# Performance work log

Hardware: AMD Instinct MI355X
Metric: run time of the kernel (lower is better)

Reference implementation:

```python
import jax, jax.numpy as jnp
import numpy as np

B, S, D, F, H, E = 4, 1024, 512, 2048, 8, 8
LN_EPS = 1e-5


def setup_inputs() -> dict:
    key = jax.random.key(0)
    ks = jax.random.split(key, 8)
    sd = 1.0 / np.sqrt(D)
    return {
        'x': jax.random.normal(ks[0], (B, S, D), jnp.float32),
        'in_proj_w': jax.random.normal(ks[1], (3 * D, D), jnp.float32) * sd,
        'in_proj_b': jnp.zeros((3 * D,), jnp.float32),
        'out_proj_w': jax.random.normal(ks[2], (D, D), jnp.float32) * sd,
        'out_proj_b': jnp.zeros((D,), jnp.float32),
        'ln1_g': jnp.ones((D,), jnp.float32),
        'ln1_b': jnp.zeros((D,), jnp.float32),
        'ln2_g': jnp.ones((D,), jnp.float32),
        'ln2_b': jnp.zeros((D,), jnp.float32),
        'router_w': jax.random.normal(ks[3], (D, E), jnp.float32) * sd,
        'wi': jax.random.normal(ks[4], (E, D, F), jnp.float32) * sd,
        'wo': jax.random.normal(ks[5], (E, F, D), jnp.float32) * (1.0 / np.sqrt(F)),
        'expert_capacity': 256,
    }


def _layernorm(x, g, b):
    mu = jnp.mean(x, axis=-1, keepdims=True)
    var = jnp.var(x, axis=-1, keepdims=True)
    return (x - mu) * jax.lax.rsqrt(var + LN_EPS) * g + b


def _mha(x, in_w, in_b, out_w, out_b):
    # torch nn.MultiheadAttention, batch_first, self-attention, no mask
    qkv = x @ in_w.T + in_b                         # [B,S,3D]
    q, k, v = jnp.split(qkv, 3, axis=-1)
    hd = D // H

    def heads(t):
        return t.reshape(B, S, H, hd).transpose(0, 2, 1, 3)  # [B,H,S,hd]

    q, k, v = heads(q), heads(k), heads(v)
    scores = jnp.einsum('bhqd,bhkd->bhqk', q, k) / np.sqrt(hd)
    attn = jax.nn.softmax(scores, axis=-1)
    o = jnp.einsum('bhqk,bhkd->bhqd', attn, v)
    o = o.transpose(0, 2, 1, 3).reshape(B, S, D)
    return o @ out_w.T + out_b


def _router(x, router_w, capacity):
    # Switch-style top-1 router with per-(batch,expert) capacity
    logits = x.astype(jnp.float32) @ router_w       # [B,S,E]
    probs = jax.nn.softmax(logits, axis=-1)
    idx = jnp.argmax(probs, axis=-1)                # [B,S]
    one_hot = jax.nn.one_hot(idx, E, dtype=probs.dtype)
    pos = jnp.cumsum(one_hot, axis=1)               # position within each expert queue
    keep = one_hot * (pos <= capacity).astype(probs.dtype)
    expert_mask = keep * probs                      # dispatch mask scaled by router prob
    return expert_mask, probs, logits


def reference(x, in_proj_w, in_proj_b, out_proj_w, out_proj_b,
              ln1_g, ln1_b, ln2_g, ln2_b, router_w, wi, wo, expert_capacity):
    # self-attention block (post-norm)
    residual = x
    a = _mha(x, in_proj_w, in_proj_b, out_proj_w, out_proj_b)
    h = _layernorm(residual + a, ln1_g, ln1_b)

    # sparse MoE FFN
    expert_mask, _, router_logits = _router(h, router_w, expert_capacity)
    residual = h
    moe = jnp.zeros_like(h)
    for e in range(E):  # fixed small expert loop; masked-dense == gather/FFN/scatter
        y = jax.nn.gelu(h @ wi[e], approximate=False) @ wo[e]
        moe = moe + expert_mask[..., e:e + 1] * y

    out = _layernorm(residual + moe, ln2_g, ln2_b)
    return out, router_logits, expert_mask
```

## Files before the change

kernel.cpp:

```cpp
#include <hip/hip_runtime.h>
#include <math.h>

#define SEQ 1024
#define NTOK 4096
#define DM 512
#define FF 2048
#define NE 8

typedef __attribute__((ext_vector_type(8))) short bf16x8;
typedef __attribute__((ext_vector_type(4))) float f32x4;

__device__ __forceinline__ short f2bf(float f) {
  unsigned u = __float_as_uint(f);
  unsigned r = (u + 0x7FFFu + ((u >> 16) & 1u)) >> 16;
  return (short)r;
}
__device__ __forceinline__ float bf2f(short h) {
  return __uint_as_float(((unsigned)(unsigned short)h) << 16);
}

#define GLOAD_LDS16(g, l) __builtin_amdgcn_global_load_lds( \
    (const __attribute__((address_space(1))) void*)(g),     \
    (__attribute__((address_space(3))) void*)(l), 16, 0, 0)

__global__ __launch_bounds__(256) void split_kernel(const float* __restrict__ src,
    short* __restrict__ hi, short* __restrict__ lo) {
  const size_t base = ((size_t)blockIdx.x * 256 + threadIdx.x) * 8;
  float4 v0 = *reinterpret_cast<const float4*>(src + base);
  float4 v1 = *reinterpret_cast<const float4*>(src + base + 4);
  short h[8]; short l[8];
  float v[8] = {v0.x, v0.y, v0.z, v0.w, v1.x, v1.y, v1.z, v1.w};
#pragma unroll
  for (int i = 0; i < 8; ++i) {
    h[i] = f2bf(v[i]);
    l[i] = f2bf(v[i] - bf2f(h[i]));
  }
  *reinterpret_cast<short4*>(hi + base)     = make_short4(h[0], h[1], h[2], h[3]);
  *reinterpret_cast<short4*>(hi + base + 4) = make_short4(h[4], h[5], h[6], h[7]);
  *reinterpret_cast<short4*>(lo + base)     = make_short4(l[0], l[1], l[2], l[3]);
  *reinterpret_cast<short4*>(lo + base + 4) = make_short4(l[4], l[5], l[6], l[7]);
}

template<int BNF>
__global__ __launch_bounds__(256) void gemm_split(const short* __restrict__ Ah, const short* __restrict__ Al,
    const short* __restrict__ Bh, const short* __restrict__ Bl,
    const float* __restrict__ bias, const float* __restrict__ resid, float* __restrict__ C,
    int N, int K) {
  constexpr int BN = 32 * BNF;
  __shared__ __align__(16) short AsH[128 * 32];
  __shared__ __align__(16) short AsL[128 * 32];
  __shared__ __align__(16) short BsH[BN * 32];
  __shared__ __align__(16) short BsL[BN * 32];
  const int n0 = blockIdx.x * BN, m0 = blockIdx.y * 128;
  const int tid = threadIdx.x;
  const int lane = tid & 63, w = tid >> 6;
  const int quad = lane >> 4, l15 = lane & 15;
  const int wm = (w & 1) * 64, wn = (w >> 1) * 16 * BNF;
  const int sr = tid >> 2, sc = (tid & 3) * 8;
  const short* Ahp = Ah + (size_t)(m0 + sr) * K;
  const short* Alp = Al + (size_t)(m0 + sr) * K;
  const short* Bhp = Bh + (size_t)(n0 + sr) * K;
  const short* Blp = Bl + (size_t)(n0 + sr) * K;
  f32x4 acc[4][BNF];
#pragma unroll
  for (int i = 0; i < 4; ++i)
#pragma unroll
    for (int j = 0; j < BNF; ++j) acc[i][j] = (f32x4){0.f, 0.f, 0.f, 0.f};
  for (int kt = 0; kt < K; kt += 32) {
    GLOAD_LDS16(Ahp + kt + sc,                  &AsH[tid * 8]);
    GLOAD_LDS16(Ahp + (size_t)64 * K + kt + sc, &AsH[2048 + tid * 8]);
    GLOAD_LDS16(Alp + kt + sc,                  &AsL[tid * 8]);
    GLOAD_LDS16(Alp + (size_t)64 * K + kt + sc, &AsL[2048 + tid * 8]);
    GLOAD_LDS16(Bhp + kt + sc,                  &BsH[tid * 8]);
    GLOAD_LDS16(Blp + kt + sc,                  &BsL[tid * 8]);
    if (BNF == 4) {
      GLOAD_LDS16(Bhp + (size_t)64 * K + kt + sc, &BsH[2048 + tid * 8]);
      GLOAD_LDS16(Blp + (size_t)64 * K + kt + sc, &BsL[2048 + tid * 8]);
    }
    __syncthreads();
    bf16x8 ah[4], al[4], bh[BNF], bl[BNF];
#pragma unroll
    for (int i = 0; i < 4; ++i) {
      ah[i] = *reinterpret_cast<const bf16x8*>(&AsH[(wm + i * 16 + l15) * 32 + quad * 8]);
      al[i] = *reinterpret_cast<const bf16x8*>(&AsL[(wm + i * 16 + l15) * 32 + quad * 8]);
    }
#pragma unroll
    for (int j = 0; j < BNF; ++j) {
      bh[j] = *reinterpret_cast<const bf16x8*>(&BsH[(wn + j * 16 + l15) * 32 + quad * 8]);
      bl[j] = *reinterpret_cast<const bf16x8*>(&BsL[(wn + j * 16 + l15) * 32 + quad * 8]);
    }
#pragma unroll
    for (int i = 0; i < 4; ++i)
#pragma unroll
      for (int j = 0; j < BNF; ++j) {
        acc[i][j] = __builtin_amdgcn_mfma_f32_16x16x32_bf16(al[i], bh[j], acc[i][j], 0, 0, 0);
        acc[i][j] = __builtin_amdgcn_mfma_f32_16x16x32_bf16(ah[i], bl[j], acc[i][j], 0, 0, 0);
        acc[i][j] = __builtin_amdgcn_mfma_f32_16x16x32_bf16(ah[i], bh[j], acc[i][j], 0, 0, 0);
      }
    __syncthreads();
  }
#pragma unroll
  for (int i = 0; i < 4; ++i) {
#pragma unroll
    for (int reg = 0; reg < 4; ++reg) {
      const int row = m0 + wm + i * 16 + quad * 4 + reg;
#pragma unroll
      for (int j = 0; j < BNF; ++j) {
        const int col = n0 + wn + j * 16 + l15;
        float v = acc[i][j][reg] + bias[col];
        if (resid) v += resid[(size_t)row * N + col];
        C[(size_t)row * N + col] = v;
      }
    }
  }
}

__global__ __launch_bounds__(256) void gemm_split_qkv(const short* __restrict__ Ah, const short* __restrict__ Al,
    const short* __restrict__ Bh, const short* __restrict__ Bl, const float* __restrict__ bias,
    short* __restrict__ qkh, short* __restrict__ qkl, short* __restrict__ vh, short* __restrict__ vl) {
  const int K = DM;
  __shared__ __align__(16) short AsH[128 * 32];
  __shared__ __align__(16) short AsL[128 * 32];
  __shared__ __align__(16) short BsH[64 * 32];
  __shared__ __align__(16) short BsL[64 * 32];
  const int n0 = blockIdx.x * 64, m0 = blockIdx.y * 128;
  const int tid = threadIdx.x;
  const int lane = tid & 63, w = tid >> 6;
  const int quad = lane >> 4, l15 = lane & 15;
  const int wm = (w & 1) * 64, wn = (w >> 1) * 32;
  const int sr = tid >> 2, sc = (tid & 3) * 8;
  const short* Ahp = Ah + (size_t)(m0 + sr) * K;
  const short* Alp = Al + (size_t)(m0 + sr) * K;
  const short* Bhp = Bh + (size_t)(n0 + sr) * K;
  const short* Blp = Bl + (size_t)(n0 + sr) * K;
  f32x4 acc[4][2];
#pragma unroll
  for (int i = 0; i < 4; ++i)
#pragma unroll
    for (int j = 0; j < 2; ++j) acc[i][j] = (f32x4){0.f, 0.f, 0.f, 0.f};
  for (int kt = 0; kt < K; kt += 32) {
    GLOAD_LDS16(Ahp + kt + sc,                  &AsH[tid * 8]);
    GLOAD_LDS16(Ahp + (size_t)64 * K + kt + sc, &AsH[2048 + tid * 8]);
    GLOAD_LDS16(Alp + kt + sc,                  &AsL[tid * 8]);
    GLOAD_LDS16(Alp + (size_t)64 * K + kt + sc, &AsL[2048 + tid * 8]);
    GLOAD_LDS16(Bhp + kt + sc,                  &BsH[tid * 8]);
    GLOAD_LDS16(Blp + kt + sc,                  &BsL[tid * 8]);
    __syncthreads();
    bf16x8 ah[4], al[4], bh[2], bl[2];
#pragma unroll
    for (int i = 0; i < 4; ++i) {
      ah[i] = *reinterpret_cast<const bf16x8*>(&AsH[(wm + i * 16 + l15) * 32 + quad * 8]);
      al[i] = *reinterpret_cast<const bf16x8*>(&AsL[(wm + i * 16 + l15) * 32 + quad * 8]);
    }
#pragma unroll
    for (int j = 0; j < 2; ++j) {
      bh[j] = *reinterpret_cast<const bf16x8*>(&BsH[(wn + j * 16 + l15) * 32 + quad * 8]);
      bl[j] = *reinterpret_cast<const bf16x8*>(&BsL[(wn + j * 16 + l15) * 32 + quad * 8]);
    }
#pragma unroll
    for (int i = 0; i < 4; ++i)
#pragma unroll
      for (int j = 0; j < 2; ++j) {
        acc[i][j] = __builtin_amdgcn_mfma_f32_16x16x32_bf16(al[i], bh[j], acc[i][j], 0, 0, 0);
        acc[i][j] = __builtin_amdgcn_mfma_f32_16x16x32_bf16(ah[i], bl[j], acc[i][j], 0, 0, 0);
        acc[i][j] = __builtin_amdgcn_mfma_f32_16x16x32_bf16(ah[i], bh[j], acc[i][j], 0, 0, 0);
      }
    __syncthreads();
  }
  if (n0 < 1024) {
#pragma unroll
    for (int i = 0; i < 4; ++i) {
#pragma unroll
      for (int reg = 0; reg < 4; ++reg) {
        const int row = m0 + wm + i * 16 + quad * 4 + reg;
#pragma unroll
        for (int j = 0; j < 2; ++j) {
          const int col = n0 + wn + j * 16 + l15;
          float v = acc[i][j][reg] + bias[col];
          short hv = f2bf(v);
          size_t ad = (size_t)row * 1024 + col;
          qkh[ad] = hv;
          qkl[ad] = f2bf(v - bf2f(hv));
        }
      }
    }
  } else {
#pragma unroll
    for (int i = 0; i < 4; ++i) {
      const int row0 = m0 + wm + i * 16 + quad * 4;
      const int bb = row0 >> 10, s0 = row0 & 1023;
#pragma unroll
      for (int j = 0; j < 2; ++j) {
        const int col = n0 + wn + j * 16 + l15;
        const int c2 = col - 1024;
        const int hhd = c2 >> 6, d = c2 & 63;
        const float bc = bias[col];
        float v0 = acc[i][j][0] + bc, v1 = acc[i][j][1] + bc, v2 = acc[i][j][2] + bc, v3 = acc[i][j][3] + bc;
        short4 hv = make_short4(f2bf(v0), f2bf(v1), f2bf(v2), f2bf(v3));
        short4 lv = make_short4(f2bf(v0 - bf2f(hv.x)), f2bf(v1 - bf2f(hv.y)),
                                f2bf(v2 - bf2f(hv.z)), f2bf(v3 - bf2f(hv.w)));
        size_t ad = ((size_t)(bb * 8 + hhd) * 64 + d) * 1024 + s0;
        *reinterpret_cast<short4*>(vh + ad) = hv;
        *reinterpret_cast<short4*>(vl + ad) = lv;
      }
    }
  }
}

__global__ __launch_bounds__(256) void attn_mfma(const short* __restrict__ qkh, const short* __restrict__ qkl,
    const short* __restrict__ vth, const short* __restrict__ vtl,
    float* __restrict__ opart, float* __restrict__ ml) {
  const int qt = blockIdx.x, hh = blockIdx.y;
  const int b = blockIdx.z >> 1, ks = blockIdx.z & 1;
  __shared__ __align__(16) short Qh[4096], Ql[4096], Kh[4096], Kl[4096], Vh[4096], Vl[4096];
  const int tid = threadIdx.x;
  const int lane = tid & 63, w = tid >> 6;
  const int quad = lane >> 4, l15 = lane & 15;
  const int tok0 = b * SEQ + qt * 64;
  const int srow = tid >> 2, schunk = (tid & 3) * 8;
  {
    const size_t qa = (size_t)(tok0 + srow) * 1024 + hh * 64 + schunk;
    GLOAD_LDS16(qkh + qa,      &Qh[tid * 8]);
    GLOAD_LDS16(qkh + qa + 32, &Qh[2048 + tid * 8]);
    GLOAD_LDS16(qkl + qa,      &Ql[tid * 8]);
    GLOAD_LDS16(qkl + qa + 32, &Ql[2048 + tid * 8]);
  }
  __syncthreads();
  bf16x8 qfh[2], qfl[2];
#pragma unroll
  for (int kk = 0; kk < 2; ++kk) {
    qfh[kk] = *reinterpret_cast<const bf16x8*>(&Qh[kk * 2048 + (w * 16 + l15) * 32 + quad * 8]);
    qfl[kk] = *reinterpret_cast<const bf16x8*>(&Ql[kk * 2048 + (w * 16 + l15) * 32 + quad * 8]);
  }
  f32x4 oacc[4];
  float m_run[4], l_run[4];
#pragma unroll
  for (int r = 0; r < 4; ++r) { oacc[r] = (f32x4){0.f, 0.f, 0.f, 0.f}; m_run[r] = -1e30f; l_run[r] = 0.f; }
  const size_t kbase = (size_t)(b * SEQ) * 1024 + 512 + hh * 64;
  const size_t vbase = (size_t)(b * 8 + hh) * 64 * 1024;
  for (int kc = ks * 8; kc < ks * 8 + 8; ++kc) {
    const size_t ka = kbase + (size_t)(kc * 64 + srow) * 1024 + schunk;
    GLOAD_LDS16(qkh + ka,      &Kh[tid * 8]);
    GLOAD_LDS16(qkh + ka + 32, &Kh[2048 + tid * 8]);
    GLOAD_LDS16(qkl + ka,      &Kl[tid * 8]);
    GLOAD_LDS16(qkl + ka + 32, &Kl[2048 + tid * 8]);
    const size_t va = vbase + (size_t)srow * 1024 + kc * 64 + schunk;
    GLOAD_LDS16(vth + va,      &Vh[tid * 8]);
    GLOAD_LDS16(vth + va + 32, &Vh[2048 + tid * 8]);
    GLOAD_LDS16(vtl + va,      &Vl[tid * 8]);
    GLOAD_LDS16(vtl + va + 32, &Vl[2048 + tid * 8]);
    __syncthreads();
    f32x4 s[4];
#pragma unroll
    for (int j = 0; j < 4; ++j) s[j] = (f32x4){0.f, 0.f, 0.f, 0.f};
#pragma unroll
    for (int kk = 0; kk < 2; ++kk)
#pragma unroll
      for (int j = 0; j < 4; ++j) {
        bf16x8 kfh = *reinterpret_cast<const bf16x8*>(&Kh[kk * 2048 + (j * 16 + l15) * 32 + quad * 8]);
        bf16x8 kfl = *reinterpret_cast<const bf16x8*>(&Kl[kk * 2048 + (j * 16 + l15) * 32 + quad * 8]);
        s[j] = __builtin_amdgcn_mfma_f32_16x16x32_bf16(qfl[kk], kfh, s[j], 0, 0, 0);
        s[j] = __builtin_amdgcn_mfma_f32_16x16x32_bf16(qfh[kk], kfl, s[j], 0, 0, 0);
        s[j] = __builtin_amdgcn_mfma_f32_16x16x32_bf16(qfh[kk], kfh, s[j], 0, 0, 0);
      }
    __syncthreads();
    float pv[4][4], alpha[4];
#pragma unroll
    for (int reg = 0; reg < 4; ++reg) {
      float mc = fmaxf(fmaxf(s[0][reg], s[1][reg]), fmaxf(s[2][reg], s[3][reg]));
#pragma unroll
      for (int msk = 1; msk < 16; msk <<= 1) mc = fmaxf(mc, __shfl_xor(mc, msk, 64));
      mc *= 0.125f;
      float mn = fmaxf(m_run[reg], mc);
      alpha[reg] = expf(m_run[reg] - mn);
      m_run[reg] = mn;
      float pl = 0.f;
#pragma unroll
      for (int j = 0; j < 4; ++j) { float pp = expf(s[j][reg] * 0.125f - mn); pv[j][reg] = pp; pl += pp; }
#pragma unroll
      for (int msk = 1; msk < 16; msk <<= 1) pl += __shfl_xor(pl, msk, 64);
      l_run[reg] = l_run[reg] * alpha[reg] + pl;
    }
#pragma unroll
    for (int j = 0; j < 4; ++j) {
      oacc[j][0] *= alpha[0]; oacc[j][1] *= alpha[1]; oacc[j][2] *= alpha[2]; oacc[j][3] *= alpha[3];
    }
#pragma unroll
    for (int j = 0; j < 4; ++j) {
      const int cad = (j >> 1) * 2048 + (j & 1) * 16 + l15;
#pragma unroll
      for (int reg = 0; reg < 4; ++reg) {
        const int ad = cad + (w * 16 + quad * 4 + reg) * 32;
        float p = pv[j][reg];
        short hp = f2bf(p);
        Kh[ad] = hp;
        Kl[ad] = f2bf(p - bf2f(hp));
      }
    }
#pragma unroll
    for (int kk = 0; kk < 2; ++kk) {
      bf16x8 pfh = *reinterpret_cast<const bf16x8*>(&Kh[kk * 2048 + (w * 16 + l15) * 32 + quad * 8]);
      bf16x8 pfl = *reinterpret_cast<const bf16x8*>(&Kl[kk * 2048 + (w * 16 + l15) * 32 + quad * 8]);
#pragma unroll
      for (int j = 0; j < 4; ++j) {
        bf16x8 vfh = *reinterpret_cast<const bf16x8*>(&Vh[kk * 2048 + (j * 16 + l15) * 32 + quad * 8]);
        bf16x8 vfl = *reinterpret_cast<const bf16x8*>(&Vl[kk * 2048 + (j * 16 + l15) * 32 + quad * 8]);
        oacc[j] = __builtin_amdgcn_mfma_f32_16x16x32_bf16(pfl, vfh, oacc[j], 0, 0, 0);
        oacc[j] = __builtin_amdgcn_mfma_f32_16x16x32_bf16(pfh, vfl, oacc[j], 0, 0, 0);
        oacc[j] = __builtin_amdgcn_mfma_f32_16x16x32_bf16(pfh, vfh, oacc[j], 0, 0, 0);
      }
    }
    __syncthreads();
  }
  float* op = opart + (size_t)ks * 2097152;
#pragma unroll
  for (int reg = 0; reg < 4; ++reg) {
    const int rloc = w * 16 + quad * 4 + reg;
#pragma unroll
    for (int j = 0; j < 4; ++j)
      op[(size_t)(tok0 + rloc) * 512 + hh * 64 + j * 16 + l15] = oacc[j][reg];
    if (l15 == 0) {
      size_t mli = (((size_t)ks * 32 + b * 8 + hh) * 1024 + qt * 64 + rloc) * 2;
      ml[mli] = m_run[reg];
      ml[mli + 1] = l_run[reg];
    }
  }
}

__global__ __launch_bounds__(64) void combine_attn(const float* __restrict__ opart, const float* __restrict__ ml,
    short* __restrict__ oh, short* __restrict__ ol) {
  const int t = blockIdx.x;
  const int b = t >> 10, s = t & 1023;
  const int tid = threadIdx.x;
#pragma unroll
  for (int hh = 0; hh < 8; ++hh) {
    size_t mli = (((size_t)(b * 8 + hh)) * 1024 + s) * 2;
    float m0 = ml[mli], l0 = ml[mli + 1];
    float m1 = ml[65536 + mli], l1 = ml[65536 + mli + 1];
    float mm = fmaxf(m0, m1);
    float a0 = expf(m0 - mm), a1 = expf(m1 - mm);
    float inv = 1.f / (l0 * a0 + l1 * a1);
    size_t ad = (size_t)t * 512 + hh * 64 + tid;
    float v = (opart[ad] * a0 + opart[2097152 + ad] * a1) * inv;
    short hv = f2bf(v);
    oh[ad] = hv;
    ol[ad] = f2bf(v - bf2f(hv));
  }
}

__global__ __launch_bounds__(64) void ln_router(const float* __restrict__ r1,
    const float* __restrict__ g, const float* __restrict__ bta, const float* __restrict__ rw,
    float* __restrict__ h, float* __restrict__ rlog, float* __restrict__ probs, int* __restrict__ am) {
  const int t = blockIdx.x, tid = threadIdx.x;
  const size_t base = (size_t)t * DM + tid * 8;
  float4 v0 = *reinterpret_cast<const float4*>(r1 + base);
  float4 v1 = *reinterpret_cast<const float4*>(r1 + base + 4);
  float s = v0.x+v0.y+v0.z+v0.w + v1.x+v1.y+v1.z+v1.w;
  float q = v0.x*v0.x+v0.y*v0.y+v0.z*v0.z+v0.w*v0.w + v1.x*v1.x+v1.y*v1.y+v1.z*v1.z+v1.w*v1.w;
#pragma unroll
  for (int m = 1; m < 64; m <<= 1) { s += __shfl_xor(s, m, 64); q += __shfl_xor(q, m, 64); }
  float mean = s * (1.0f/512.0f);
  float var = q * (1.0f/512.0f) - mean * mean;
  float rs = rsqrtf(var + 1e-5f);
  float4 g0 = *reinterpret_cast<const float4*>(g + tid*8);
  float4 g1 = *reinterpret_cast<const float4*>(g + tid*8 + 4);
  float4 b0 = *reinterpret_cast<const float4*>(bta + tid*8);
  float4 b1 = *reinterpret_cast<const float4*>(bta + tid*8 + 4);
  float hv[8];
  hv[0] = (v0.x-mean)*rs*g0.x+b0.x; hv[1] = (v0.y-mean)*rs*g0.y+b0.y;
  hv[2] = (v0.z-mean)*rs*g0.z+b0.z; hv[3] = (v0.w-mean)*rs*g0.w+b0.w;
  hv[4] = (v1.x-mean)*rs*g1.x+b1.x; hv[5] = (v1.y-mean)*rs*g1.y+b1.y;
  hv[6] = (v1.z-mean)*rs*g1.z+b1.z; hv[7] = (v1.w-mean)*rs*g1.w+b1.w;
  *reinterpret_cast<float4*>(h + base)     = make_float4(hv[0], hv[1], hv[2], hv[3]);
  *reinterpret_cast<float4*>(h + base + 4) = make_float4(hv[4], hv[5], hv[6], hv[7]);
  float lg[8] = {0.f,0.f,0.f,0.f,0.f,0.f,0.f,0.f};
  const float* rwp = rw + tid * 64;
#pragma unroll
  for (int r = 0; r < 8; ++r) {
    float4 w0 = *reinterpret_cast<const float4*>(rwp + r * 8);
    float4 w1 = *reinterpret_cast<const float4*>(rwp + r * 8 + 4);
    float hr = hv[r];
    lg[0] += hr * w0.x; lg[1] += hr * w0.y; lg[2] += hr * w0.z; lg[3] += hr * w0.w;
    lg[4] += hr * w1.x; lg[5] += hr * w1.y; lg[6] += hr * w1.z; lg[7] += hr * w1.w;
  }
#pragma unroll
  for (int m = 1; m < 64; m <<= 1) {
#pragma unroll
    for (int e = 0; e < 8; ++e) lg[e] += __shfl_xor(lg[e], m, 64);
  }
  int best = 0; float bv = lg[0];
#pragma unroll
  for (int e = 1; e < 8; ++e) if (lg[e] > bv) { bv = lg[e]; best = e; }
  float se = 0.f;
#pragma unroll
  for (int e = 0; e < 8; ++e) se += expf(lg[e] - bv);
  float inv = 1.f / se;
  if (tid < 8) {
    rlog[t * 8 + tid] = lg[tid];
    probs[t * 8 + tid] = expf(lg[tid] - bv) * inv;
  }
  if (tid == 0) am[t] = best;
}

__global__ __launch_bounds__(64) void ln2_kernel(const float* __restrict__ x, const float* __restrict__ add,
    const int* __restrict__ pos, const int* __restrict__ capp,
    const float* __restrict__ g, const float* __restrict__ bta, float* __restrict__ y) {
  const int t = blockIdx.x, tid = threadIdx.x;
  const size_t base = (size_t)t * DM + tid * 8;
  float4 v0 = *reinterpret_cast<const float4*>(x + base);
  float4 v1 = *reinterpret_cast<const float4*>(x + base + 4);
  if (pos[t] <= *capp) {
    float4 a0 = *reinterpret_cast<const float4*>(add + base);
    float4 a1 = *reinterpret_cast<const float4*>(add + base + 4);
    v0.x += a0.x; v0.y += a0.y; v0.z += a0.z; v0.w += a0.w;
    v1.x += a1.x; v1.y += a1.y; v1.z += a1.z; v1.w += a1.w;
  }
  float s = v0.x+v0.y+v0.z+v0.w + v1.x+v1.y+v1.z+v1.w;
  float q = v0.x*v0.x+v0.y*v0.y+v0.z*v0.z+v0.w*v0.w + v1.x*v1.x+v1.y*v1.y+v1.z*v1.z+v1.w*v1.w;
#pragma unroll
  for (int m = 1; m < 64; m <<= 1) { s += __shfl_xor(s, m, 64); q += __shfl_xor(q, m, 64); }
  float mean = s * (1.0f/512.0f);
  float var = q * (1.0f/512.0f) - mean * mean;
  float rs = rsqrtf(var + 1e-5f);
  float4 g0 = *reinterpret_cast<const float4*>(g + tid*8);
  float4 g1 = *reinterpret_cast<const float4*>(g + tid*8 + 4);
  float4 b0 = *reinterpret_cast<const float4*>(bta + tid*8);
  float4 b1 = *reinterpret_cast<const float4*>(bta + tid*8 + 4);
  float4 o0 = make_float4((v0.x-mean)*rs*g0.x+b0.x, (v0.y-mean)*rs*g0.y+b0.y,
                          (v0.z-mean)*rs*g0.z+b0.z, (v0.w-mean)*rs*g0.w+b0.w);
  float4 o1 = make_float4((v1.x-mean)*rs*g1.x+b1.x, (v1.y-mean)*rs*g1.y+b1.y,
                          (v1.z-mean)*rs*g1.z+b1.z, (v1.w-mean)*rs*g1.w+b1.w);
  *reinterpret_cast<float4*>(y + base) = o0;
  *reinterpret_cast<float4*>(y + base + 4) = o1;
}

__global__ __launch_bounds__(256) void scan_kernel(const int* __restrict__ am, const float* __restrict__ probs,
    const int* __restrict__ capp, float* __restrict__ emask, int* __restrict__ pos, int* __restrict__ cnt) {
  const int bx = blockIdx.x;
  const int b = bx >> 3, e = bx & 7;
  const int tid = threadIdx.x;
  const int cap = *capp;
  __shared__ int arr[256];
  const int s_base = tid * 4;
  int f[4], incl[4];
  int c = 0;
#pragma unroll
  for (int i = 0; i < 4; ++i) {
    f[i] = (am[b * SEQ + s_base + i] == e) ? 1 : 0;
    c += f[i]; incl[i] = c;
  }
  arr[tid] = c;
  __syncthreads();
  for (int off = 1; off < 256; off <<= 1) {
    int v = (tid >= off) ? arr[tid - off] : 0;
    __syncthreads();
    arr[tid] += v;
    __syncthreads();
  }
  int excl = arr[tid] - c;
  int tot = arr[255];
#pragma unroll
  for (int i = 0; i < 4; ++i) {
    int token = b * SEQ + s_base + i;
    int p = excl + incl[i];
    bool kept = f[i] && (p <= cap);
    emask[(size_t)token * NE + e] = kept ? probs[token * NE + e] : 0.f;
    if (f[i]) pos[token] = p;
  }
  if (tid == 0) cnt[bx] = (tot < cap) ? tot : cap;
}

__global__ __launch_bounds__(64) void offsets_kernel(const int* __restrict__ cnt, int* __restrict__ offbe,
    int* __restrict__ total) {
  int e = threadIdx.x;
  if (e < NE) {
    int run = 0;
    for (int b = 0; b < 4; ++b) { offbe[b * NE + e] = run; run += cnt[b * NE + e]; }
    total[e] = run;
  }
}

__global__ __launch_bounds__(256) void transpose_bf16(const float* __restrict__ W, short* __restrict__ Wt,
    int K, int N) {
  __shared__ float T[32][33];
  const float* We = W + (size_t)blockIdx.z * K * N;
  short* Wte = Wt + (size_t)blockIdx.z * K * N;
  const int k0 = blockIdx.y * 32, n0 = blockIdx.x * 32;
  const int r = threadIdx.x >> 3, c4 = (threadIdx.x & 7) * 4;
  float4 v = *reinterpret_cast<const float4*>(&We[(size_t)(k0 + r) * N + n0 + c4]);
  T[r][c4+0] = v.x; T[r][c4+1] = v.y; T[r][c4+2] = v.z; T[r][c4+3] = v.w;
  __syncthreads();
  short4 o;
  o.x = f2bf(T[c4+0][r]); o.y = f2bf(T[c4+1][r]); o.z = f2bf(T[c4+2][r]); o.w = f2bf(T[c4+3][r]);
  *reinterpret_cast<short4*>(&Wte[(size_t)(n0 + r) * K + k0 + c4]) = o;
}

__global__ __launch_bounds__(128) void gather_kernel(const float* __restrict__ h, const int* __restrict__ am,
    const int* __restrict__ pos, const int* __restrict__ capp, const int* __restrict__ offbe,
    const float* __restrict__ probs, short* __restrict__ Gb, int* __restrict__ tok, float* __restrict__ mscale) {
  const int t = blockIdx.x;
  const int b = t >> 10;
  const int e = am[t];
  const int p = pos[t];
  if (p > *capp) return;
  const int slot = offbe[b * NE + e] + p - 1;
  const int idx = e * 1024 + slot;
  if (threadIdx.x == 0) { tok[idx] = t; mscale[idx] = probs[t * NE + e]; }
  float4 v = *reinterpret_cast<const float4*>(h + (size_t)t * DM + threadIdx.x * 4);
  short4 o; o.x = f2bf(v.x); o.y = f2bf(v.y); o.z = f2bf(v.z); o.w = f2bf(v.w);
  *reinterpret_cast<short4*>(Gb + (size_t)idx * DM + threadIdx.x * 4) = o;
}

__global__ __launch_bounds__(256) void ffn1_mfma(const short* __restrict__ Gb, const short* __restrict__ wi_t,
    short* __restrict__ mid, const int* __restrict__ total) {
  const int e = blockIdx.z;
  const int tot = total[e];
  const int m0 = blockIdx.y * 128;
  if (m0 >= tot) return;
  const int n0 = blockIdx.x * 128;
  __shared__ __align__(16) short As[128 * 32];
  __shared__ __align__(16) short Bs[128 * 32];
  const short* A = Gb + ((size_t)e * 1024 + m0) * DM;
  const short* B = wi_t + (size_t)e * FF * DM + (size_t)n0 * DM;
  const int tid = threadIdx.x;
  const int lane = tid & 63, w = tid >> 6;
  const int quad = lane >> 4, l15 = lane & 15;
  const int wm = (w & 1) * 64, wn = (w >> 1) * 64;
  const int sr = tid >> 2, sc = (tid & 3) * 8;
  f32x4 acc[4][4];
#pragma unroll
  for (int i = 0; i < 4; ++i)
#pragma unroll
    for (int j = 0; j < 4; ++j) acc[i][j] = (f32x4){0.f, 0.f, 0.f, 0.f};
  for (int kt = 0; kt < DM; kt += 32) {
    GLOAD_LDS16(A + (size_t)sr * DM + kt + sc,        &As[tid * 8]);
    GLOAD_LDS16(A + (size_t)(sr + 64) * DM + kt + sc, &As[2048 + tid * 8]);
    GLOAD_LDS16(B + (size_t)sr * DM + kt + sc,        &Bs[tid * 8]);
    GLOAD_LDS16(B + (size_t)(sr + 64) * DM + kt + sc, &Bs[2048 + tid * 8]);
    __syncthreads();
    bf16x8 a[4], b[4];
#pragma unroll
    for (int i = 0; i < 4; ++i) a[i] = *reinterpret_cast<const bf16x8*>(&As[(wm + i * 16 + l15) * 32 + quad * 8]);
#pragma unroll
    for (int j = 0; j < 4; ++j) b[j] = *reinterpret_cast<const bf16x8*>(&Bs[(wn + j * 16 + l15) * 32 + quad * 8]);
#pragma unroll
    for (int i = 0; i < 4; ++i)
#pragma unroll
      for (int j = 0; j < 4; ++j)
        acc[i][j] = __builtin_amdgcn_mfma_f32_16x16x32_bf16(a[i], b[j], acc[i][j], 0, 0, 0);
    __syncthreads();
  }
#pragma unroll
  for (int i = 0; i < 4; ++i) {
#pragma unroll
    for (int reg = 0; reg < 4; ++reg) {
      int row = m0 + wm + i * 16 + quad * 4 + reg;
      short* outr = mid + ((size_t)e * 1024 + row) * FF;
#pragma unroll
      for (int j = 0; j < 4; ++j) {
        float v = acc[i][j][reg];
        float gl = 0.5f * v * (1.f + erff(v * 0.70710678118654752f));
        outr[n0 + wn + j * 16 + l15] = f2bf(gl);
      }
    }
  }
}

__global__ __launch_bounds__(256) void ffn2_mfma(const short* __restrict__ mid, const short* __restrict__ wo_t,
    const int* __restrict__ tok, const float* __restrict__ mscale, const int* __restrict__ total,
    float* __restrict__ moebuf) {
  const int e = blockIdx.z;
  const int tot = total[e];
  const int m0 = blockIdx.y * 128;
  if (m0 >= tot) return;
  const int n0 = blockIdx.x * 128;
  __shared__ __align__(16) short As[128 * 32];
  __shared__ __align__(16) short Bs[128 * 32];
  const short* A = mid + ((size_t)e * 1024 + m0) * FF;
  const short* B = wo_t + (size_t)e * DM * FF + (size_t)n0 * FF;
  const int tid = threadIdx.x;
  const int lane = tid & 63, w = tid >> 6;
  const int quad = lane >> 4, l15 = lane & 15;
  const int wm = (w & 1) * 64, wn = (w >> 1) * 64;
  const int sr = tid >> 2, sc = (tid & 3) * 8;
  f32x4 acc[4][4];
#pragma unroll
  for (int i = 0; i < 4; ++i)
#pragma unroll
    for (int j = 0; j < 4; ++j) acc[i][j] = (f32x4){0.f, 0.f, 0.f, 0.f};
  for (int kt = 0; kt < FF; kt += 32) {
    GLOAD_LDS16(A + (size_t)sr * FF + kt + sc,        &As[tid * 8]);
    GLOAD_LDS16(A + (size_t)(sr + 64) * FF + kt + sc, &As[2048 + tid * 8]);
    GLOAD_LDS16(B + (size_t)sr * FF + kt + sc,        &Bs[tid * 8]);
    GLOAD_LDS16(B + (size_t)(sr + 64) * FF + kt + sc, &Bs[2048 + tid * 8]);
    __syncthreads();
    bf16x8 a[4], b[4];
#pragma unroll
    for (int i = 0; i < 4; ++i) a[i] = *reinterpret_cast<const bf16x8*>(&As[(wm + i * 16 + l15) * 32 + quad * 8]);
#pragma unroll
    for (int j = 0; j < 4; ++j) b[j] = *reinterpret_cast<const bf16x8*>(&Bs[(wn + j * 16 + l15) * 32 + quad * 8]);
#pragma unroll
    for (int i = 0; i < 4; ++i)
#pragma unroll
      for (int j = 0; j < 4; ++j)
        acc[i][j] = __builtin_amdgcn_mfma_f32_16x16x32_bf16(a[i], b[j], acc[i][j], 0, 0, 0);
    __syncthreads();
  }
#pragma unroll
  for (int i = 0; i < 4; ++i) {
#pragma unroll
    for (int reg = 0; reg < 4; ++reg) {
      int slot = m0 + wm + i * 16 + quad * 4 + reg;
      if (slot < tot) {
        int idx = e * 1024 + slot;
        int t = tok[idx];
        float scv = mscale[idx];
        float* outr = moebuf + (size_t)t * DM + n0 + wn;
#pragma unroll
        for (int j = 0; j < 4; ++j) outr[j * 16 + l15] = scv * acc[i][j][reg];
      }
    }
  }
}

extern "C" void kernel_launch(void* const* d_in, const int* in_sizes, int n_in,
                              void* d_out, int out_size, void* d_ws, size_t ws_size,
                              hipStream_t stream) {
  const float* x     = (const float*)d_in[0];
  const float* in_w  = (const float*)d_in[1];
  const float* in_b  = (const float*)d_in[2];
  const float* out_w = (const float*)d_in[3];
  const float* out_b = (const float*)d_in[4];
  const float* ln1g  = (const float*)d_in[5];
  const float* ln1b  = (const float*)d_in[6];
  const float* ln2g  = (const float*)d_in[7];
  const float* ln2b  = (const float*)d_in[8];
  const float* rw    = (const float*)d_in[9];
  const float* wi    = (const float*)d_in[10];
  const float* wo    = (const float*)d_in[11];
  const int*   capp  = (const int*)d_in[12];

  float* ws = (float*)d_ws;
  short* qkh  = (short*)ws;
  short* qkl  = (short*)(ws + 2097152);
  short* vth  = (short*)(ws + 4194304);
  short* vtl  = (short*)(ws + 5242880);
  short* Gb16 = (short*)ws;
  short* wi_t = (short*)(ws + 2097152);
  float* moebuf = ws + 6291456;
  float* r1     = ws + 8388608;
  float* h      = ws + 10485760;
  float* probs  = ws + 12582912;
  short* wo_t   = (short*)(ws + 12615680);
  float* opart  = ws + 16809984;
  float* mlbuf  = ws + 16809984 + 4194304;
  short* mid16  = (short*)(ws + 16809984);
  float* mscale = ws + 25198592;
  int* am    = (int*)(ws + 25206784);
  int* pos   = am + NTOK;
  int* cnt   = pos + NTOK;
  int* offbe = cnt + 32;
  int* total = offbe + 32;
  int* tok   = total + 8;
  short* sAh = (short*)(ws + 25231360);
  short* sAl = sAh + 2097152;
  short* sBh = sAl + 2097152;
  short* sBl = sBh + 786432;

  float* out   = (float*)d_out;
  float* rlog  = out + 2097152;
  float* emask = rlog + 32768;

  split_kernel<<<1024, 256, 0, stream>>>(x, sAh, sAl);
  split_kernel<<<384, 256, 0, stream>>>(in_w, sBh, sBl);
  gemm_split_qkv<<<dim3(24, 32), 256, 0, stream>>>(sAh, sAl, sBh, sBl, in_b, qkh, qkl, vth, vtl);
  attn_mfma<<<dim3(16, 8, 8), 256, 0, stream>>>(qkh, qkl, vth, vtl, opart, mlbuf);
  combine_attn<<<NTOK, 64, 0, stream>>>(opart, mlbuf, sAh, sAl);
  split_kernel<<<128, 256, 0, stream>>>(out_w, sBh, sBl);
  gemm_split<2><<<dim3(8, 32), 256, 0, stream>>>(sAh, sAl, sBh, sBl, out_b, x, r1, DM, DM);
  transpose_bf16<<<dim3(64, 16, 8), 256, 0, stream>>>(wi, wi_t, DM, FF);
  transpose_bf16<<<dim3(16, 64, 8), 256, 0, stream>>>(wo, wo_t, FF, DM);
  ln_router<<<NTOK, 64, 0, stream>>>(r1, ln1g, ln1b, rw, h, rlog, probs, am);
  scan_kernel<<<32, 256, 0, stream>>>(am, probs, capp, emask, pos, cnt);
  offsets_kernel<<<1, 64, 0, stream>>>(cnt, offbe, total);
  gather_kernel<<<NTOK, 128, 0, stream>>>(h, am, pos, capp, offbe, probs, Gb16, tok, mscale);
  ffn1_mfma<<<dim3(16, 8, 8), 256, 0, stream>>>(Gb16, wi_t, mid16, total);
  ffn2_mfma<<<dim3(4, 8, 8), 256, 0, stream>>>(mid16, wo_t, tok, mscale, total, moebuf);
  ln2_kernel<<<NTOK, 64, 0, stream>>>(h, moebuf, pos, capp, ln2g, ln2b, out);
}
```

Before: 372.2 us.

## Merge small launches, drop offsets kernel, load Q directly, shrink GEMM tiles

Merges the three split launches into one, and the two weight transposes into one launch. Removes the offsets kernel by having the consumers compute prefix sums from the counts inline. Attention loads Q fragments directly from global memory instead of staging them through LDS. The out-projection GEMM and ffn2 use narrower N tiles so more blocks run. Together these cut launch count and raise occupancy, at the cost of some redundant per-block index arithmetic and less reuse per tile.

New measurement: 349.2 us. -6.2%, faster.

```diff
diff --git a/kernel.cpp b/kernel.cpp
--- a/kernel.cpp
+++ b/kernel.cpp
@@ -23,9 +23,16 @@
     (const __attribute__((address_space(1))) void*)(g),     \
     (__attribute__((address_space(3))) void*)(l), 16, 0, 0)
 
-__global__ __launch_bounds__(256) void split_kernel(const float* __restrict__ src,
-    short* __restrict__ hi, short* __restrict__ lo) {
-  const size_t base = ((size_t)blockIdx.x * 256 + threadIdx.x) * 8;
+__global__ __launch_bounds__(256) void split3_kernel(
+    const float* __restrict__ x, short* __restrict__ xh, short* __restrict__ xl,
+    const float* __restrict__ w1, short* __restrict__ w1h, short* __restrict__ w1l,
+    const float* __restrict__ w2, short* __restrict__ w2h, short* __restrict__ w2l) {
+  const int bid = blockIdx.x;
+  const float* src; short* hi; short* lo; size_t off;
+  if (bid < 1024)      { src = x;  hi = xh;  lo = xl;  off = (size_t)bid * 2048; }
+  else if (bid < 1408) { src = w1; hi = w1h; lo = w1l; off = (size_t)(bid - 1024) * 2048; }
+  else                 { src = w2; hi = w2h; lo = w2l; off = (size_t)(bid - 1408) * 2048; }
+  const size_t base = off + threadIdx.x * 8;
   float4 v0 = *reinterpret_cast<const float4*>(src + base);
   float4 v1 = *reinterpret_cast<const float4*>(src + base + 4);
   short h[8]; short l[8];
@@ -71,8 +78,10 @@
     GLOAD_LDS16(Ahp + (size_t)64 * K + kt + sc, &AsH[2048 + tid * 8]);
     GLOAD_LDS16(Alp + kt + sc,                  &AsL[tid * 8]);
     GLOAD_LDS16(Alp + (size_t)64 * K + kt + sc, &AsL[2048 + tid * 8]);
-    GLOAD_LDS16(Bhp + kt + sc,                  &BsH[tid * 8]);
-    GLOAD_LDS16(Blp + kt + sc,                  &BsL[tid * 8]);
+    if (BNF >= 2 || tid < 128) {
+      GLOAD_LDS16(Bhp + kt + sc,                &BsH[tid * 8]);
+      GLOAD_LDS16(Blp + kt + sc,                &BsL[tid * 8]);
+    }
     if (BNF == 4) {
       GLOAD_LDS16(Bhp + (size_t)64 * K + kt + sc, &BsH[2048 + tid * 8]);
       GLOAD_LDS16(Blp + (size_t)64 * K + kt + sc, &BsL[2048 + tid * 8]);
@@ -212,25 +221,19 @@
     float* __restrict__ opart, float* __restrict__ ml) {
   const int qt = blockIdx.x, hh = blockIdx.y;
   const int b = blockIdx.z >> 1, ks = blockIdx.z & 1;
-  __shared__ __align__(16) short Qh[4096], Ql[4096], Kh[4096], Kl[4096], Vh[4096], Vl[4096];
+  __shared__ __align__(16) short Kh[4096], Kl[4096], Vh[4096], Vl[4096];
   const int tid = threadIdx.x;
   const int lane = tid & 63, w = tid >> 6;
   const int quad = lane >> 4, l15 = lane & 15;
   const int tok0 = b * SEQ + qt * 64;
   const int srow = tid >> 2, schunk = (tid & 3) * 8;
+  bf16x8 qfh[2], qfl[2];
   {
-    const size_t qa = (size_t)(tok0 + srow) * 1024 + hh * 64 + schunk;
-    GLOAD_LDS16(qkh + qa,      &Qh[tid * 8]);
-    GLOAD_LDS16(qkh + qa + 32, &Qh[2048 + tid * 8]);
-    GLOAD_LDS16(qkl + qa,      &Ql[tid * 8]);
-    GLOAD_LDS16(qkl + qa + 32, &Ql[2048 + tid * 8]);
-  }
-  __syncthreads();
-  bf16x8 qfh[2], qfl[2];
-#pragma unroll
-  for (int kk = 0; kk < 2; ++kk) {
-    qfh[kk] = *reinterpret_cast<const bf16x8*>(&Qh[kk * 2048 + (w * 16 + l15) * 32 + quad * 8]);
-    qfl[kk] = *reinterpret_cast<const bf16x8*>(&Ql[kk * 2048 + (w * 16 + l15) * 32 + quad * 8]);
+    const size_t qa = (size_t)(tok0 + w * 16 + l15) * 1024 + hh * 64 + quad * 8;
+    qfh[0] = *reinterpret_cast<const bf16x8*>(qkh + qa);
+    qfh[1] = *reinterpret_cast<const bf16x8*>(qkh + qa + 32);
+    qfl[0] = *reinterpret_cast<const bf16x8*>(qkl + qa);
+    qfl[1] = *reinterpret_cast<const bf16x8*>(qkl + qa + 32);
   }
   f32x4 oacc[4];
   float m_run[4], l_run[4];
@@ -470,40 +473,35 @@
   if (tid == 0) cnt[bx] = (tot < cap) ? tot : cap;
 }
 
-__global__ __launch_bounds__(64) void offsets_kernel(const int* __restrict__ cnt, int* __restrict__ offbe,
-    int* __restrict__ total) {
-  int e = threadIdx.x;
-  if (e < NE) {
-    int run = 0;
-    for (int b = 0; b < 4; ++b) { offbe[b * NE + e] = run; run += cnt[b * NE + e]; }
-    total[e] = run;
-  }
-}
-
-__global__ __launch_bounds__(256) void transpose_bf16(const float* __restrict__ W, short* __restrict__ Wt,
-    int K, int N) {
+__global__ __launch_bounds__(256) void transpose2_bf16(const float* __restrict__ wi, short* __restrict__ wi_t,
+    const float* __restrict__ wo, short* __restrict__ wo_t) {
   __shared__ float T[32][33];
-  const float* We = W + (size_t)blockIdx.z * K * N;
-  short* Wte = Wt + (size_t)blockIdx.z * K * N;
-  const int k0 = blockIdx.y * 32, n0 = blockIdx.x * 32;
+  const int z = blockIdx.z;
+  const float* W; short* Wt; int K, N, k0, n0;
+  if (z < 8) { W = wi + (size_t)z * DM * FF;      Wt = wi_t + (size_t)z * DM * FF;
+               K = DM; N = FF; k0 = blockIdx.y * 32; n0 = blockIdx.x * 32; }
+  else       { W = wo + (size_t)(z - 8) * FF * DM; Wt = wo_t + (size_t)(z - 8) * FF * DM;
+               K = FF; N = DM; k0 = blockIdx.x * 32; n0 = blockIdx.y * 32; }
   const int r = threadIdx.x >> 3, c4 = (threadIdx.x & 7) * 4;
-  float4 v = *reinterpret_cast<const float4*>(&We[(size_t)(k0 + r) * N + n0 + c4]);
+  float4 v = *reinterpret_cast<const float4*>(&W[(size_t)(k0 + r) * N + n0 + c4]);
   T[r][c4+0] = v.x; T[r][c4+1] = v.y; T[r][c4+2] = v.z; T[r][c4+3] = v.w;
   __syncthreads();
   short4 o;
   o.x = f2bf(T[c4+0][r]); o.y = f2bf(T[c4+1][r]); o.z = f2bf(T[c4+2][r]); o.w = f2bf(T[c4+3][r]);
-  *reinterpret_cast<short4*>(&Wte[(size_t)(n0 + r) * K + k0 + c4]) = o;
+  *reinterpret_cast<short4*>(&Wt[(size_t)(n0 + r) * K + k0 + c4]) = o;
 }
 
 __global__ __launch_bounds__(128) void gather_kernel(const float* __restrict__ h, const int* __restrict__ am,
-    const int* __restrict__ pos, const int* __restrict__ capp, const int* __restrict__ offbe,
+    const int* __restrict__ pos, const int* __restrict__ capp, const int* __restrict__ cnt,
     const float* __restrict__ probs, short* __restrict__ Gb, int* __restrict__ tok, float* __restrict__ mscale) {
   const int t = blockIdx.x;
   const int b = t >> 10;
   const int e = am[t];
   const int p = pos[t];
   if (p > *capp) return;
-  const int slot = offbe[b * NE + e] + p - 1;
+  int off = 0;
+  for (int b2 = 0; b2 < b; ++b2) off += cnt[b2 * 8 + e];
+  const int slot = off + p - 1;
   const int idx = e * 1024 + slot;
   if (threadIdx.x == 0) { tok[idx] = t; mscale[idx] = probs[t * NE + e]; }
   float4 v = *reinterpret_cast<const float4*>(h + (size_t)t * DM + threadIdx.x * 4);
@@ -512,9 +510,9 @@
 }
 
 __global__ __launch_bounds__(256) void ffn1_mfma(const short* __restrict__ Gb, const short* __restrict__ wi_t,
-    short* __restrict__ mid, const int* __restrict__ total) {
+    short* __restrict__ mid, const int* __restrict__ cnt) {
   const int e = blockIdx.z;
-  const int tot = total[e];
+  const int tot = cnt[e] + cnt[8 + e] + cnt[16 + e] + cnt[24 + e];
   const int m0 = blockIdx.y * 128;
   if (m0 >= tot) return;
   const int n0 = blockIdx.x * 128;
@@ -567,42 +565,41 @@
 }
 
 __global__ __launch_bounds__(256) void ffn2_mfma(const short* __restrict__ mid, const short* __restrict__ wo_t,
-    const int* __restrict__ tok, const float* __restrict__ mscale, const int* __restrict__ total,
+    const int* __restrict__ tok, const float* __restrict__ mscale, const int* __restrict__ cnt,
     float* __restrict__ moebuf) {
   const int e = blockIdx.z;
-  const int tot = total[e];
+  const int tot = cnt[e] + cnt[8 + e] + cnt[16 + e] + cnt[24 + e];
   const int m0 = blockIdx.y * 128;
   if (m0 >= tot) return;
-  const int n0 = blockIdx.x * 128;
+  const int n0 = blockIdx.x * 64;
   __shared__ __align__(16) short As[128 * 32];
-  __shared__ __align__(16) short Bs[128 * 32];
+  __shared__ __align__(16) short Bs[64 * 32];
   const short* A = mid + ((size_t)e * 1024 + m0) * FF;
   const short* B = wo_t + (size_t)e * DM * FF + (size_t)n0 * FF;
   const int tid = threadIdx.x;
   const int lane = tid & 63, w = tid >> 6;
   const int quad = lane >> 4, l15 = lane & 15;
-  const int wm = (w & 1) * 64, wn = (w >> 1) * 64;
+  const int wm = (w & 1) * 64, wn = (w >> 1) * 32;
   const int sr = tid >> 2, sc = (tid & 3) * 8;
-  f32x4 acc[4][4];
+  f32x4 acc[4][2];
 #pragma unroll
   for (int i = 0; i < 4; ++i)
 #pragma unroll
-    for (int j = 0; j < 4; ++j) acc[i][j] = (f32x4){0.f, 0.f, 0.f, 0.f};
+    for (int j = 0; j < 2; ++j) acc[i][j] = (f32x4){0.f, 0.f, 0.f, 0.f};
   for (int kt = 0; kt < FF; kt += 32) {
     GLOAD_LDS16(A + (size_t)sr * FF + kt + sc,        &As[tid * 8]);
     GLOAD_LDS16(A + (size_t)(sr + 64) * FF + kt + sc, &As[2048 + tid * 8]);
     GLOAD_LDS16(B + (size_t)sr * FF + kt + sc,        &Bs[tid * 8]);
-    GLOAD_LDS16(B + (size_t)(sr + 64) * FF + kt + sc, &Bs[2048 + tid * 8]);
-    __syncthreads();
-    bf16x8 a[4], b[4];
+    __syncthreads();
+    bf16x8 a[4], b[2];
 #pragma unroll
     for (int i = 0; i < 4; ++i) a[i] = *reinterpret_cast<const bf16x8*>(&As[(wm + i * 16 + l15) * 32 + quad * 8]);
 #pragma unroll
-    for (int j = 0; j < 4; ++j) b[j] = *reinterpret_cast<const bf16x8*>(&Bs[(wn + j * 16 + l15) * 32 + quad * 8]);
+    for (int j = 0; j < 2; ++j) b[j] = *reinterpret_cast<const bf16x8*>(&Bs[(wn + j * 16 + l15) * 32 + quad * 8]);
 #pragma unroll
     for (int i = 0; i < 4; ++i)
 #pragma unroll
-      for (int j = 0; j < 4; ++j)
+      for (int j = 0; j < 2; ++j)
         acc[i][j] = __builtin_amdgcn_mfma_f32_16x16x32_bf16(a[i], b[j], acc[i][j], 0, 0, 0);
     __syncthreads();
   }
@@ -617,7 +614,7 @@
         float scv = mscale[idx];
         float* outr = moebuf + (size_t)t * DM + n0 + wn;
 #pragma unroll
-        for (int j = 0; j < 4; ++j) outr[j * 16 + l15] = scv * acc[i][j][reg];
+        for (int j = 0; j < 2; ++j) outr[j * 16 + l15] = scv * acc[i][j][reg];
       }
     }
   }
@@ -659,32 +656,28 @@
   int* am    = (int*)(ws + 25206784);
   int* pos   = am + NTOK;
   int* cnt   = pos + NTOK;
-  int* offbe = cnt + 32;
-  int* total = offbe + 32;
-  int* tok   = total + 8;
+  int* tok   = cnt + 32;
   short* sAh = (short*)(ws + 25231360);
   short* sAl = sAh + 2097152;
   short* sBh = sAl + 2097152;
   short* sBl = sBh + 786432;
+  short* sCh = sBl + 786432;
+  short* sCl = sCh + 262144;
 
   float* out   = (float*)d_out;
   float* rlog  = out + 2097152;
   float* emask = rlog + 32768;
 
-  split_kernel<<<1024, 256, 0, stream>>>(x, sAh, sAl);
-  split_kernel<<<384, 256, 0, stream>>>(in_w, sBh, sBl);
+  split3_kernel<<<1536, 256, 0, stream>>>(x, sAh, sAl, in_w, sBh, sBl, out_w, sCh, sCl);
   gemm_split_qkv<<<dim3(24, 32), 256, 0, stream>>>(sAh, sAl, sBh, sBl, in_b, qkh, qkl, vth, vtl);
   attn_mfma<<<dim3(16, 8, 8), 256, 0, stream>>>(qkh, qkl, vth, vtl, opart, mlbuf);
   combine_attn<<<NTOK, 64, 0, stream>>>(opart, mlbuf, sAh, sAl);
-  split_kernel<<<128, 256, 0, stream>>>(out_w, sBh, sBl);
-  gemm_split<2><<<dim3(8, 32), 256, 0, stream>>>(sAh, sAl, sBh, sBl, out_b, x, r1, DM, DM);
-  transpose_bf16<<<dim3(64, 16, 8), 256, 0, stream>>>(wi, wi_t, DM, FF);
-  transpose_bf16<<<dim3(16, 64, 8), 256, 0, stream>>>(wo, wo_t, FF, DM);
+  gemm_split<1><<<dim3(16, 32), 256, 0, stream>>>(sAh, sAl, sCh, sCl, out_b, x, r1, DM, DM);
+  transpose2_bf16<<<dim3(64, 16, 16), 256, 0, stream>>>(wi, wi_t, wo, wo_t);
   ln_router<<<NTOK, 64, 0, stream>>>(r1, ln1g, ln1b, rw, h, rlog, probs, am);
   scan_kernel<<<32, 256, 0, stream>>>(am, probs, capp, emask, pos, cnt);
-  offsets_kernel<<<1, 64, 0, stream>>>(cnt, offbe, total);
-  gather_kernel<<<NTOK, 128, 0, stream>>>(h, am, pos, capp, offbe, probs, Gb16, tok, mscale);
-  ffn1_mfma<<<dim3(16, 8, 8), 256, 0, stream>>>(Gb16, wi_t, mid16, total);
-  ffn2_mfma<<<dim3(4, 8, 8), 256, 0, stream>>>(mid16, wo_t, tok, mscale, total, moebuf);
+  gather_kernel<<<NTOK, 128, 0, stream>>>(h, am, pos, capp, cnt, probs, Gb16, tok, mscale);
+  ffn1_mfma<<<dim3(16, 8, 8), 256, 0, stream>>>(Gb16, wi_t, mid16, cnt);
+  ffn2_mfma<<<dim3(8, 8, 8), 256, 0, stream>>>(mid16, wo_t, tok, mscale, cnt, moebuf);
   ln2_kernel<<<NTOK, 64, 0, stream>>>(h, moebuf, pos, capp, ln2g, ln2b, out);
 }
```
